# Kernel optimization log

Measured on AMD Instinct MI355X. Metric: run time of the kernel, lower is better.

The kernel has to match this reference:

```python
import jax, jax.numpy as jnp
import numpy as np

SEQ = 2097152   # seq_len (2^21)
IN = 4          # input_size
H = 2           # hidden_size (forced: y init is a 2-vector)
OUT = 2         # output_size


def setup_inputs() -> dict:
    key = jax.random.key(0)
    ks = jax.random.split(key, 7)
    x = jax.random.normal(ks[0], (1, SEQ, IN), jnp.float32)
    # fc1: Linear(input_size -> hidden_size)
    W1 = jax.random.normal(ks[1], (H, IN), jnp.float32) / np.sqrt(IN)
    b1 = jax.random.normal(ks[2], (H,), jnp.float32) * 0.1
    # DNNCNN cell: combines current fc1 output h_t (H,) with previous output y (H,)
    Wd = jax.random.normal(ks[3], (H, 2 * H), jnp.float32) / np.sqrt(2 * H)
    bd = jax.random.normal(ks[4], (H,), jnp.float32) * 0.1
    # fc2: Linear(hidden_size -> output_size)
    W2 = jax.random.normal(ks[5], (OUT, H), jnp.float32) / np.sqrt(H)
    b2 = jax.random.normal(ks[6], (OUT,), jnp.float32) * 0.1
    return {"x": x, "W1": W1, "b1": b1, "Wd": Wd, "bd": bd,
            "W2": W2, "b2": b2, "length": SEQ}


def reference(x, W1, b1, Wd, bd, W2, b2, length):
    # fc1 over all timesteps: (1, S, H)
    h = jnp.einsum('bsi,hi->bsh', x, W1) + b1

    # Sequential per-timestep DNNC cell: y_t = dnnc(h_t, y_{t-1}).
    # True data dependency -> lax.scan over the time axis (batch is 1).
    def step(y, h_t):
        z = jnp.concatenate([h_t, y])          # (2H,)
        y_new = jax.nn.relu(Wd @ z + bd)        # (H,)
        return y_new, y_new

    y0 = jnp.zeros((H,), dtype=x.dtype)
    _, x1 = jax.lax.scan(step, y0, h[0])        # (S, H)

    out = jax.nn.sigmoid(x1 @ W2.T + b2)        # (S, OUT)
    return out.reshape(-1, OUT)
```

## Files before the change

### kernel.cpp

```cpp
#include <hip/hip_runtime.h>
#include <math.h>


#define L_CHUNK 16
#define W_WARM  128
#define PITCH   18
#define EXT     264
#define EXT_STEPS (EXT * 16)

__global__ __launch_bounds__(256)
void rnn_fused(const float4* __restrict__ x4,
               const float* __restrict__ W1, const float* __restrict__ b1,
               const float* __restrict__ Wd, const float* __restrict__ bd,
               const float* __restrict__ W2, const float* __restrict__ b2,
               float2* __restrict__ out)
{
    __shared__ float2 tile[EXT * PITCH];
    const int tid = threadIdx.x;
    const int c0 = blockIdx.x * 256;
    const long t0 = (long)c0 * 16 - W_WARM;

    const float w100 = W1[0], w101 = W1[1], w102 = W1[2], w103 = W1[3];
    const float w110 = W1[4], w111 = W1[5], w112 = W1[6], w113 = W1[7];
    const float c10 = b1[0], c11 = b1[1];
    const float a00 = Wd[0], a01 = Wd[1], B00 = Wd[2], B01 = Wd[3];
    const float a10 = Wd[4], a11 = Wd[5], B10 = Wd[6], B11 = Wd[7];
    const float d0 = bd[0], d1 = bd[1];
    const float w200 = W2[0], w201 = W2[1], w210 = W2[2], w211 = W2[3];
    const float e0 = b2[0], e1 = b2[1];

    #pragma unroll 4
    for (int i = 0; i < 17; ++i) {
        int tl = i * 256 + tid;
        if (tl < EXT_STEPS) {
            long t = t0 + tl;
            if (t < 0) t = 0;
            float4 xv = x4[t];
            float h0 = fmaf(w100, xv.x, fmaf(w101, xv.y, fmaf(w102, xv.z, fmaf(w103, xv.w, c10))));
            float h1 = fmaf(w110, xv.x, fmaf(w111, xv.y, fmaf(w112, xv.z, fmaf(w113, xv.w, c11))));
            tile[(tl >> 4) * PITCH + (tl & 15)] = make_float2(h0, h1);
        }
    }
    __syncthreads();

    float y0 = 0.f, y1 = 0.f;
    float2 o[16];
    const int gc = c0 + tid;

    for (int g = 0; g < 9; ++g) {
        const bool live = (g == 8);
        if (!live && (gc - 8 + g) < 0) continue;
        const float4* row = (const float4*)&tile[(tid + g) * PITCH];
        float4 q[8];
        #pragma unroll
        for (int j = 0; j < 8; ++j) q[j] = row[j];
        const float2* hv = (const float2*)q;
        #pragma unroll
        for (int k = 0; k < 16; ++k) {
            float p0 = fmaf(a00, hv[k].x, fmaf(a01, hv[k].y, d0));
            float p1 = fmaf(a10, hv[k].x, fmaf(a11, hv[k].y, d1));
            float z0 = fmaf(B00, y0, fmaf(B01, y1, p0));
            float z1 = fmaf(B10, y0, fmaf(B11, y1, p1));
            y0 = fmaxf(z0, 0.f);
            y1 = fmaxf(z1, 0.f);
            if (live) {
                float u0 = fmaf(w200, y0, fmaf(w201, y1, e0));
                float u1 = fmaf(w210, y0, fmaf(w211, y1, e1));
                o[k] = make_float2(1.f / (1.f + __expf(-u0)),
                                   1.f / (1.f + __expf(-u1)));
            }
        }
    }
    __syncthreads();

    #pragma unroll
    for (int k = 0; k < 16; ++k)
        tile[tid * PITCH + k] = o[k];
    __syncthreads();

    const long base = (long)blockIdx.x * 4096;
    #pragma unroll 4
    for (int i = 0; i < 16; ++i) {
        int e = i * 256 + tid;
        out[base + e] = tile[(e >> 4) * PITCH + (e & 15)];
    }
}

extern "C" void kernel_launch(void* const* d_in, const int* in_sizes, int n_in,
                              void* d_out, int out_size, void* d_ws, size_t ws_size,
                              hipStream_t stream) {
    const float4* x4 = (const float4*)d_in[0];
    const float* W1v = (const float*)d_in[1];
    const float* b1v = (const float*)d_in[2];
    const float* Wdv = (const float*)d_in[3];
    const float* bdv = (const float*)d_in[4];
    const float* W2v = (const float*)d_in[5];
    const float* b2v = (const float*)d_in[6];

    const int S = in_sizes[0] / 4;
    const int nChunks = S / L_CHUNK;
    const int grid = nChunks / 256;

    rnn_fused<<<grid, 256, 0, stream>>>(x4, W1v, b1v, Wdv, bdv, W2v, b2v,
                                        (float2*)d_out);
}
```

Measured before the change: 98.56 us.

## Halve per-thread chunk length and batch all input loads before computing fc1

Each thread's chunk shrinks from 16 to 8 timesteps, which doubles the grid and the number of independent recurrence chains. The warm-up window stays at 128 steps, now spread over 16 preceding chunks. All nine float4 input loads are issued into registers before any fc1 math, to raise memory-level parallelism, and 64-bit indexing is replaced with int. The trade-off is more warm-up recurrence work per output step and more blocks re-reading overlapping halo input.

```diff
diff --git a/kernel.cpp b/kernel.cpp
--- a/kernel.cpp
+++ b/kernel.cpp
@@ -2,11 +2,12 @@
 #include <math.h>
 
 
-#define L_CHUNK 16
+#define L_CHUNK 8
 #define W_WARM  128
-#define PITCH   18
-#define EXT     264
-#define EXT_STEPS (EXT * 16)
+#define HALO    16
+#define EXT     272
+#define EXT_STEPS (EXT * L_CHUNK)
+#define PITCH   10
 
 __global__ __launch_bounds__(256)
 void rnn_fused(const float4* __restrict__ x4,
@@ -15,10 +16,10 @@
                const float* __restrict__ W2, const float* __restrict__ b2,
                float2* __restrict__ out)
 {
-    __shared__ float2 tile[EXT * PITCH];
+    __shared__ alignas(16) float2 tile[EXT * PITCH];
     const int tid = threadIdx.x;
     const int c0 = blockIdx.x * 256;
-    const long t0 = (long)c0 * 16 - W_WARM;
+    const int t0 = c0 * L_CHUNK - W_WARM;
 
     const float w100 = W1[0], w101 = W1[1], w102 = W1[2], w103 = W1[3];
     const float w110 = W1[4], w111 = W1[5], w112 = W1[6], w113 = W1[7];
@@ -29,34 +30,39 @@
     const float w200 = W2[0], w201 = W2[1], w210 = W2[2], w211 = W2[3];
     const float e0 = b2[0], e1 = b2[1];
 
-    #pragma unroll 4
-    for (int i = 0; i < 17; ++i) {
+    float4 q[9];
+    #pragma unroll
+    for (int i = 0; i < 9; ++i) {
+        int tl = i * 256 + tid;
+        if (tl > EXT_STEPS - 1) tl = EXT_STEPS - 1;
+        int t = t0 + tl;
+        if (t < 0) t = 0;
+        q[i] = x4[t];
+    }
+    #pragma unroll
+    for (int i = 0; i < 9; ++i) {
         int tl = i * 256 + tid;
         if (tl < EXT_STEPS) {
-            long t = t0 + tl;
-            if (t < 0) t = 0;
-            float4 xv = x4[t];
+            float4 xv = q[i];
             float h0 = fmaf(w100, xv.x, fmaf(w101, xv.y, fmaf(w102, xv.z, fmaf(w103, xv.w, c10))));
             float h1 = fmaf(w110, xv.x, fmaf(w111, xv.y, fmaf(w112, xv.z, fmaf(w113, xv.w, c11))));
-            tile[(tl >> 4) * PITCH + (tl & 15)] = make_float2(h0, h1);
+            tile[(tl >> 3) * PITCH + (tl & 7)] = make_float2(h0, h1);
         }
     }
     __syncthreads();
 
     float y0 = 0.f, y1 = 0.f;
-    float2 o[16];
-    const int gc = c0 + tid;
+    float2 o[L_CHUNK];
 
-    for (int g = 0; g < 9; ++g) {
-        const bool live = (g == 8);
-        if (!live && (gc - 8 + g) < 0) continue;
+    for (int g = 0; g < HALO + 1; ++g) {
+        const bool live = (g == HALO);
+        if (!live && (c0 + tid + g - HALO) < 0) continue;
         const float4* row = (const float4*)&tile[(tid + g) * PITCH];
-        float4 q[8];
+        float4 r0 = row[0], r1 = row[1], r2 = row[2], r3 = row[3];
+        float4 rr[4] = {r0, r1, r2, r3};
+        const float2* hv = (const float2*)rr;
         #pragma unroll
-        for (int j = 0; j < 8; ++j) q[j] = row[j];
-        const float2* hv = (const float2*)q;
-        #pragma unroll
-        for (int k = 0; k < 16; ++k) {
+        for (int k = 0; k < L_CHUNK; ++k) {
             float p0 = fmaf(a00, hv[k].x, fmaf(a01, hv[k].y, d0));
             float p1 = fmaf(a10, hv[k].x, fmaf(a11, hv[k].y, d1));
             float z0 = fmaf(B00, y0, fmaf(B01, y1, p0));
@@ -74,15 +80,15 @@
     __syncthreads();
 
     #pragma unroll
-    for (int k = 0; k < 16; ++k)
+    for (int k = 0; k < L_CHUNK; ++k)
         tile[tid * PITCH + k] = o[k];
     __syncthreads();
 
-    const long base = (long)blockIdx.x * 4096;
-    #pragma unroll 4
-    for (int i = 0; i < 16; ++i) {
+    const int base = blockIdx.x * (256 * L_CHUNK);
+    #pragma unroll
+    for (int i = 0; i < L_CHUNK; ++i) {
         int e = i * 256 + tid;
-        out[base + e] = tile[(e >> 4) * PITCH + (e & 15)];
+        out[base + e] = tile[(e >> 3) * PITCH + (e & 7)];
     }
 }
 
```

After: 100.5 us. About the same (+2.0%).
